# Performance work log

Hardware: AMD Instinct MI355X
Metric: run time of the kernel (lower is better)

The kernel has to match this reference:

```python
import jax, jax.numpy as jnp
import numpy as np

EPS = 1e-05
EPS_SQRT = EPS ** 0.5


def setup_inputs() -> dict:
    key = jax.random.key(0)
    x = jax.random.normal(key, (4, 2048, 4096), dtype=jnp.float32)
    weight = jnp.ones((4096,), dtype=jnp.float32)
    bias = jnp.zeros((4096,), dtype=jnp.float32)
    return {"x": x, "weight": weight, "bias": bias}


def _sign_nz(v):
    # sign() with 0 mapped to +1 (matches torch code: x_sign[x_sign==0]=1)
    s = jnp.sign(v)
    return jnp.where(s == 0, 1.0, s)


def _layer_normal_norm(x, weight, bias):
    # standardize over last dim (biased variance, correction=0)
    mean = jnp.mean(x, axis=-1, keepdims=True)
    var = jnp.var(x, axis=-1, keepdims=True)
    xs = (x - mean) / jnp.sqrt(var + EPS)

    x_sign = _sign_nz(xs)
    x_abs = jnp.abs(xs)
    l1p = jnp.log1p(x_abs)

    # Newton estimate of lambda (order 2)
    s1 = jnp.mean(x_sign * l1p, axis=-1, keepdims=True)
    d = (1.0 + x_abs) * l1p - x_abs
    dvar = 2.0 * jnp.mean(xs * d, axis=-1, keepdims=True)
    g1 = 0.5 * dvar - s1

    dmean = jnp.mean(d, axis=-1, keepdims=True)
    d_sub_sq = jnp.square(d - dmean)
    p1 = (1.0 + x_abs) * jnp.square(l1p) - 2.0 * d
    d2 = x_sign * p1
    d2var = 2.0 * jnp.mean(xs * d2 + d_sub_sq, axis=-1, keepdims=True)
    g2 = -0.5 * jnp.square(dvar) + 0.5 * d2var

    lmbda = 1.0 - g1 / (g2 + EPS_SQRT)  # broadcasts to full [B,S,D]

    # power transform
    eta = 1.0 + x_sign * (lmbda - 1.0)
    eta_sign = jax.lax.stop_gradient(_sign_nz(eta))
    exponent = eta + eta_sign * EPS_SQRT
    x_tr1 = (x_sign / exponent) * (jnp.power(1.0 + x_abs, exponent) - 1.0)
    x_tr2 = x_sign * l1p
    mask = jax.lax.stop_gradient(jnp.abs(eta) <= EPS_SQRT)
    x_tr = jnp.where(mask, x_tr2, x_tr1)

    # eval mode: no additive noise (self.training == False)
    return x_tr * weight + bias


def reference(x, weight, bias):
    return _layer_normal_norm(x, weight, bias)
```

## Files before the change

### kernel.cpp

```cpp
#include <hip/hip_runtime.h>
#include <math.h>

#define D 4096
#define NW 4
#define NT (64 * NW)
#define EPS 1e-5f
#define EPS_SQRT 3.16227766016837933e-3f
#define LN2 0.69314718055994531f

__global__ __launch_bounds__(NT, 4) void lnn_kernel(const float* __restrict__ x,
                                                    const float* __restrict__ w,
                                                    const float* __restrict__ b,
                                                    float* __restrict__ out,
                                                    int rows) {
    const int lane = threadIdx.x & 63;
    const int wv   = threadIdx.x >> 6;
    const int row  = blockIdx.x * NW + wv;
    if (row >= rows) return;

    const float4* x4 = (const float4*)(x + (size_t)row * D);

    float v[64];
#pragma unroll
    for (int c = 0; c < 16; ++c) {
        float4 f = x4[c * 64 + lane];
        v[c*4+0] = f.x; v[c*4+1] = f.y; v[c*4+2] = f.z; v[c*4+3] = f.w;
    }

    const float inv_d = 1.f / (float)D;

    float s = 0.f, s2 = 0.f;
#pragma unroll
    for (int i = 0; i < 64; ++i) { s += v[i]; s2 = fmaf(v[i], v[i], s2); }
#pragma unroll
    for (int m = 32; m > 0; m >>= 1) {
        s  += __shfl_xor(s,  m, 64);
        s2 += __shfl_xor(s2, m, 64);
    }
    const float mean = s * inv_d;
    const float var  = s2 * inv_d - mean * mean;
    const float rstd = rsqrtf(var + EPS);
    const float nm   = -mean * rstd;

    float s1 = 0.f, sxd = 0.f, sd = 0.f, sd2 = 0.f, sxd2 = 0.f;
#pragma unroll
    for (int i = 0; i < 64; ++i) {
        float xs   = fmaf(v[i], rstd, nm);
        float ab   = fabsf(xs);
        float onea = 1.f + ab;
        float L2   = __builtin_amdgcn_logf(onea);
        float sv   = copysignf(L2, xs);
        v[i] = sv;
        s1 += sv;
        float l  = L2 * LN2;
        float dd = fmaf(onea, l, -ab);
        sxd = fmaf(xs, dd, sxd);
        sd += dd;
        sd2 = fmaf(dd, dd, sd2);
        float p1 = fmaf(onea, l * l, -(dd + dd));
        sxd2 = fmaf(ab, p1, sxd2);
    }
#pragma unroll
    for (int m = 32; m > 0; m >>= 1) {
        s1   += __shfl_xor(s1,   m, 64);
        sxd  += __shfl_xor(sxd,  m, 64);
        sd   += __shfl_xor(sd,   m, 64);
        sd2  += __shfl_xor(sd2,  m, 64);
        sxd2 += __shfl_xor(sxd2, m, 64);
    }

    const float s1m   = s1 * (inv_d * LN2);
    const float dvar  = 2.f * sxd * inv_d;
    const float g1    = 0.5f * dvar - s1m;
    const float dmean = sd * inv_d;
    const float vard  = sd2 * inv_d - dmean * dmean;
    const float d2var = 2.f * (sxd2 * inv_d + vard);
    const float g2    = -0.5f * dvar * dvar + 0.5f * d2var;
    const float lm    = 1.f - g1 * __builtin_amdgcn_rcpf(g2 + EPS_SQRT);

    const float eta_p = lm;
    const float eta_n = 2.f - lm;
    const float ep = eta_p + ((eta_p >= 0.f) ? EPS_SQRT : -EPS_SQRT);
    const float en = eta_n + ((eta_n >= 0.f) ? EPS_SQRT : -EPS_SQRT);
    const bool  mp = fabsf(eta_p) <= EPS_SQRT;
    const bool  mn = fabsf(eta_n) <= EPS_SQRT;
    const float rp =  __builtin_amdgcn_rcpf(ep);
    const float rn = -__builtin_amdgcn_rcpf(en);

    float* orow = out + (size_t)row * D;
    const float4* w4 = (const float4*)w;
    const float4* b4 = (const float4*)b;

    if (!(mp || mn)) {
#pragma unroll
        for (int c = 0; c < 16; ++c) {
            float4 wf = w4[c * 64 + lane];
            float4 bf = b4[c * 64 + lane];
            float wa[4] = {wf.x, wf.y, wf.z, wf.w};
            float ba[4] = {bf.x, bf.y, bf.z, bf.w};
            float oa[4];
#pragma unroll
            for (int j = 0; j < 4; ++j) {
                float sv = v[c*4 + j];
                bool pos = (sv >= 0.f);
                float L2 = fabsf(sv);
                float e  = pos ? ep : en;
                float re = pos ? rp : rn;
                float tr = fmaf(re, __builtin_amdgcn_exp2f(e * L2), -re);
                oa[j] = fmaf(tr, wa[j], ba[j]);
            }
            float4 o = {oa[0], oa[1], oa[2], oa[3]};
            ((float4*)orow)[c * 64 + lane] = o;
        }
    } else {
#pragma unroll
        for (int c = 0; c < 16; ++c) {
            float4 wf = w4[c * 64 + lane];
            float4 bf = b4[c * 64 + lane];
            float wa[4] = {wf.x, wf.y, wf.z, wf.w};
            float ba[4] = {bf.x, bf.y, bf.z, bf.w};
            float oa[4];
#pragma unroll
            for (int j = 0; j < 4; ++j) {
                float sv = v[c*4 + j];
                bool pos = (sv >= 0.f);
                float L2 = fabsf(sv);
                float e  = pos ? ep : en;
                float re = pos ? rp : rn;
                bool  m  = pos ? mp : mn;
                float tr1 = fmaf(re, __builtin_amdgcn_exp2f(e * L2), -re);
                float tr2 = sv * LN2;
                float tr  = m ? tr2 : tr1;
                oa[j] = fmaf(tr, wa[j], ba[j]);
            }
            float4 o = {oa[0], oa[1], oa[2], oa[3]};
            ((float4*)orow)[c * 64 + lane] = o;
        }
    }
}

extern "C" void kernel_launch(void* const* d_in, const int* in_sizes, int n_in,
                              void* d_out, int out_size, void* d_ws, size_t ws_size,
                              hipStream_t stream) {
    const float* x = (const float*)d_in[0];
    const float* w = (const float*)d_in[1];
    const float* b = (const float*)d_in[2];
    float* out = (float*)d_out;
    const int rows = in_sizes[0] / D;
    const int nblocks = (rows + NW - 1) / NW;
    lnn_kernel<<<dim3(nblocks), dim3(NT), 0, stream>>>(x, w, b, out, rows);
}
```

Measured before the change: 274.1 us.

## Re-read row from memory each pass instead of caching 64 values in registers

Drops the 64-float per-thread register cache of the row and reloads x from global memory in each of the three passes, recomputing the normalization and log in the output pass. Launch bounds rise to 8 blocks per CU so more waves can be resident and hide memory latency. In exchange each row is read three times (the 16KB row should mostly hit L2/cache) and one extra log per element is computed.

```diff
diff --git a/kernel.cpp b/kernel.cpp
--- a/kernel.cpp
+++ b/kernel.cpp
@@ -8,7 +8,7 @@
 #define EPS_SQRT 3.16227766016837933e-3f
 #define LN2 0.69314718055994531f
 
-__global__ __launch_bounds__(NT, 4) void lnn_kernel(const float* __restrict__ x,
+__global__ __launch_bounds__(NT, 8) void lnn_kernel(const float* __restrict__ x,
                                                     const float* __restrict__ w,
                                                     const float* __restrict__ b,
                                                     float* __restrict__ out,
@@ -19,19 +19,16 @@
     if (row >= rows) return;
 
     const float4* x4 = (const float4*)(x + (size_t)row * D);
-
-    float v[64];
-#pragma unroll
-    for (int c = 0; c < 16; ++c) {
-        float4 f = x4[c * 64 + lane];
-        v[c*4+0] = f.x; v[c*4+1] = f.y; v[c*4+2] = f.z; v[c*4+3] = f.w;
-    }
-
     const float inv_d = 1.f / (float)D;
 
     float s = 0.f, s2 = 0.f;
 #pragma unroll
-    for (int i = 0; i < 64; ++i) { s += v[i]; s2 = fmaf(v[i], v[i], s2); }
+    for (int c = 0; c < 16; ++c) {
+        float4 f = x4[c * 64 + lane];
+        float e0[4] = {f.x, f.y, f.z, f.w};
+#pragma unroll
+        for (int j = 0; j < 4; ++j) { s += e0[j]; s2 = fmaf(e0[j], e0[j], s2); }
+    }
 #pragma unroll
     for (int m = 32; m > 0; m >>= 1) {
         s  += __shfl_xor(s,  m, 64);
@@ -44,21 +41,24 @@
 
     float s1 = 0.f, sxd = 0.f, sd = 0.f, sd2 = 0.f, sxd2 = 0.f;
 #pragma unroll
-    for (int i = 0; i < 64; ++i) {
-        float xs   = fmaf(v[i], rstd, nm);
-        float ab   = fabsf(xs);
-        float onea = 1.f + ab;
-        float L2   = __builtin_amdgcn_logf(onea);
-        float sv   = copysignf(L2, xs);
-        v[i] = sv;
-        s1 += sv;
-        float l  = L2 * LN2;
-        float dd = fmaf(onea, l, -ab);
-        sxd = fmaf(xs, dd, sxd);
-        sd += dd;
-        sd2 = fmaf(dd, dd, sd2);
-        float p1 = fmaf(onea, l * l, -(dd + dd));
-        sxd2 = fmaf(ab, p1, sxd2);
+    for (int c = 0; c < 16; ++c) {
+        float4 f = x4[c * 64 + lane];
+        float e0[4] = {f.x, f.y, f.z, f.w};
+#pragma unroll
+        for (int j = 0; j < 4; ++j) {
+            float xs   = fmaf(e0[j], rstd, nm);
+            float ab   = fabsf(xs);
+            float onea = 1.f + ab;
+            float L2   = __builtin_amdgcn_logf(onea);
+            s1 += copysignf(L2, xs);
+            float l  = L2 * LN2;
+            float dd = fmaf(onea, l, -ab);
+            sxd = fmaf(xs, dd, sxd);
+            sd += dd;
+            sd2 = fmaf(dd, dd, sd2);
+            float p1 = fmaf(onea, l * l, -(dd + dd));
+            sxd2 = fmaf(ab, p1, sxd2);
+        }
     }
 #pragma unroll
     for (int m = 32; m > 0; m >>= 1) {
@@ -94,16 +94,18 @@
     if (!(mp || mn)) {
 #pragma unroll
         for (int c = 0; c < 16; ++c) {
+            float4 f  = x4[c * 64 + lane];
             float4 wf = w4[c * 64 + lane];
             float4 bf = b4[c * 64 + lane];
+            float e0[4] = {f.x, f.y, f.z, f.w};
             float wa[4] = {wf.x, wf.y, wf.z, wf.w};
             float ba[4] = {bf.x, bf.y, bf.z, bf.w};
             float oa[4];
 #pragma unroll
             for (int j = 0; j < 4; ++j) {
-                float sv = v[c*4 + j];
-                bool pos = (sv >= 0.f);
-                float L2 = fabsf(sv);
+                float xs = fmaf(e0[j], rstd, nm);
+                float L2 = __builtin_amdgcn_logf(1.f + fabsf(xs));
+                bool pos = (xs >= 0.f);
                 float e  = pos ? ep : en;
                 float re = pos ? rp : rn;
                 float tr = fmaf(re, __builtin_amdgcn_exp2f(e * L2), -re);
@@ -115,21 +117,23 @@
     } else {
 #pragma unroll
         for (int c = 0; c < 16; ++c) {
+            float4 f  = x4[c * 64 + lane];
             float4 wf = w4[c * 64 + lane];
             float4 bf = b4[c * 64 + lane];
+            float e0[4] = {f.x, f.y, f.z, f.w};
             float wa[4] = {wf.x, wf.y, wf.z, wf.w};
             float ba[4] = {bf.x, bf.y, bf.z, bf.w};
             float oa[4];
 #pragma unroll
             for (int j = 0; j < 4; ++j) {
-                float sv = v[c*4 + j];
-                bool pos = (sv >= 0.f);
-                float L2 = fabsf(sv);
+                float xs = fmaf(e0[j], rstd, nm);
+                float L2 = __builtin_amdgcn_logf(1.f + fabsf(xs));
+                bool pos = (xs >= 0.f);
                 float e  = pos ? ep : en;
                 float re = pos ? rp : rn;
                 bool  m  = pos ? mp : mn;
                 float tr1 = fmaf(re, __builtin_amdgcn_exp2f(e * L2), -re);
-                float tr2 = sv * LN2;
+                float tr2 = copysignf(L2 * LN2, xs);
                 float tr  = m ? tr2 : tr1;
                 oa[j] = fmaf(tr, wa[j], ba[j]);
             }
```

New measurement: 318.0 us. 16.0% more time.
